# Optimization experiments

Measured on AMD Instinct MI355X. Metric: run time of the kernel, lower is better.

The kernel has to match this reference:

```python
import jax, jax.numpy as jnp
import numpy as np

B, N, C, H = 4, 2048, 384, 8
HD = C // H  # 48; divisible by 6 so RoPE3D splits into three even-sized chunks
ROPE_BASE = 100.0  # RoPE3D(100)


def _rope1d(x, p):
    # x: [B,H,N,d], p: [B,N] integer positions
    d = x.shape[-1]
    inv = 1.0 / (ROPE_BASE ** (jnp.arange(0, d, 2, dtype=jnp.float32) / d))  # [d/2]
    ang = p[:, None, :, None].astype(jnp.float32) * inv                      # [B,1,N,d/2]
    ang = jnp.concatenate([ang, ang], axis=-1)                               # [B,1,N,d]
    cos, sin = jnp.cos(ang), jnp.sin(ang)
    x1, x2 = jnp.split(x, 2, axis=-1)
    return x * cos + jnp.concatenate([-x2, x1], axis=-1) * sin


def _rope3d(x, pos):
    # x: [B,H,N,D], pos: [B,N,3]; rotate each D/3 chunk by one spatial axis
    parts = jnp.split(x, 3, axis=-1)
    return jnp.concatenate([_rope1d(parts[i], pos[..., i]) for i in range(3)], axis=-1)


def setup_inputs() -> dict:
    key = jax.random.key(0)
    ks = jax.random.split(key, 9)
    T = B * N
    s = 1.0 / np.sqrt(C).astype(np.float32)
    offs = jnp.arange(1, B + 1, dtype=jnp.int32) * N  # equal-length segments
    return {
        "query": jax.random.normal(ks[0], (T, C), jnp.float32),
        "key": jax.random.normal(ks[1], (T, C), jnp.float32),
        "value": jax.random.normal(ks[2], (T, C), jnp.float32),
        "Wq": jax.random.normal(ks[3], (C, C), jnp.float32) * s,
        "bq": jnp.zeros((C,), jnp.float32),
        "Wk": jax.random.normal(ks[4], (C, C), jnp.float32) * s,
        "bk": jnp.zeros((C,), jnp.float32),
        "Wv": jax.random.normal(ks[5], (C, C), jnp.float32) * s,
        "bv": jnp.zeros((C,), jnp.float32),
        "Wo": jax.random.normal(ks[6], (C, C), jnp.float32) * s,
        "bo": jnp.zeros((C,), jnp.float32),
        "qpos": jax.random.randint(ks[7], (T, 3), 0, 100),
        "kpos": jax.random.randint(ks[8], (T, 3), 0, 100),
        "src_point_offset": offs,
        "tgt_point_offset": offs,
    }


def reference(query, key, value, Wq, bq, Wk, bk, Wv, bv, Wo, bo,
              qpos, kpos, src_point_offset, tgt_point_offset):
    # Equal-length segments (offsets = [N,2N,...]) => the per-item python loop
    # in forward_pcd_to_pcd is exactly one batched attention over [B,N,C].
    qb = query.reshape(B, N, C)
    kb = key.reshape(B, N, C)
    vb = value.reshape(B, N, C)
    q = (qb @ Wq.T + bq).reshape(B, N, H, HD).transpose(0, 2, 1, 3)  # [B,H,N,HD]
    k = (kb @ Wk.T + bk).reshape(B, N, H, HD).transpose(0, 2, 1, 3)
    v = (vb @ Wv.T + bv).reshape(B, N, H, HD).transpose(0, 2, 1, 3)
    q = _rope3d(q, qpos.reshape(B, N, 3))
    k = _rope3d(k, kpos.reshape(B, N, 3))
    scale = 1.0 / np.sqrt(HD).astype(np.float32)
    attn = jax.nn.softmax(jnp.einsum("bhqd,bhkd->bhqk", q, k) * scale, axis=-1)
    x = jnp.einsum("bhqk,bhkd->bhqd", attn, v)  # [B,H,N,HD]
    x = x.transpose(0, 2, 1, 3).reshape(B * N, C)
    return x @ Wo.T + bo
```

## Files before the change

kernel.cpp:

```cpp
#include <hip/hip_runtime.h>
#include <hip/hip_bf16.h>
#include <math.h>


typedef __attribute__((ext_vector_type(8))) short bf16x8;
typedef __attribute__((ext_vector_type(4))) float f32x4;
typedef __attribute__((ext_vector_type(4))) short s16x4;

__device__ inline short f2bf(float f) {
    unsigned u = __float_as_uint(f);
    u += 0x7fffu + ((u >> 16) & 1u);
    return (short)(u >> 16);
}
__device__ inline unsigned pk_bf16(float a, float b) {
    __hip_bfloat162 h = __float22bfloat162_rn(make_float2(a, b));
    return *(reinterpret_cast<unsigned*>(&h));
}
__device__ inline unsigned pk2(float lo, float hi) {
    return (__float_as_uint(lo) >> 16) | (__float_as_uint(hi) & 0xffff0000u);
}
__device__ inline float bflo(unsigned u) { return __uint_as_float(u << 16); }
__device__ inline float bfhi(unsigned u) { return __uint_as_float(u & 0xffff0000u); }
__device__ inline float exp2f_fast(float x) {
#if __has_builtin(__builtin_amdgcn_exp2f)
    return __builtin_amdgcn_exp2f(x);
#else
    return exp2f(x);
#endif
}
__device__ inline float ffract(float x) {
    float r;
    asm("v_fract_f32 %0, %1" : "=v"(r) : "v"(x));
    return r;
}
__device__ inline float fsin(float x) {
    float r;
    asm("v_sin_f32 %0, %1\n\ts_nop 1" : "=v"(r) : "v"(x));
    return r;
}
__device__ inline float fcos(float x) {
    float r;
    asm("v_cos_f32 %0, %1\n\ts_nop 1" : "=v"(r) : "v"(x));
    return r;
}
__device__ inline int div48(int c) { return (c * 683) >> 15; }

__global__ __launch_bounds__(256)
void cvt_w(const float* __restrict__ w0, const float* __restrict__ w1,
           const float* __restrict__ w2, const float* __restrict__ w3,
           short* __restrict__ Wh, short* __restrict__ Wl)
{
    const float* s = blockIdx.y == 0 ? w0 : blockIdx.y == 1 ? w1
                   : blockIdx.y == 2 ? w2 : w3;
    const size_t i = (size_t)(blockIdx.x * 256 + threadIdx.x) * 4;
    const int c = (int)(i / 384);
    const int k = (int)(i % 384);
    const float4 x = *(const float4*)(s + i);
    const unsigned h01 = pk2(x.x, x.y);
    const unsigned h23 = pk2(x.z, x.w);
    const unsigned l01 = pk2(x.x - bflo(h01), x.y - bfhi(h01));
    const unsigned l23 = pk2(x.z - bflo(h23), x.w - bfhi(h23));
    const size_t off =
        ((((size_t)blockIdx.y * 24 + (c >> 4)) * 12 + (k >> 5)) * 64
         + ((k >> 3) & 3) * 16 + (c & 15)) * 8 + (k & 7);
    uint2 hv; hv.x = h01; hv.y = h23;
    uint2 lv; lv.x = l01; lv.y = l23;
    *(uint2*)(Wh + off) = hv;
    *(uint2*)(Wl + off) = lv;
}

__global__ __launch_bounds__(256, 6)
void gemm_qkv(const float* __restrict__ q_in, const float* __restrict__ k_in,
              const float* __restrict__ v_in,
              const short* __restrict__ Whp, const short* __restrict__ Wlp,
              const float* __restrict__ bq, const float* __restrict__ bk,
              const float* __restrict__ bv,
              const int* __restrict__ qpos, const int* __restrict__ kpos,
              short* __restrict__ qp0, short* __restrict__ qtb,
              short* __restrict__ kp0, short* __restrict__ ktb,
              short* __restrict__ vp)
{
    const int z = blockIdx.z;
    const float* A = z == 0 ? q_in : z == 1 ? k_in : v_in;
    const float* bias = z == 0 ? bq : z == 1 ? bk : bv;

    const int tid = threadIdx.x;
    const int wv = tid >> 6, lane = tid & 63;
    const int l15 = lane & 15, quad = lane >> 4;
    const int mb = blockIdx.x * 32;
    const int nbl = wv * 32;
    const int n0 = blockIdx.y * 128;

    const int tbase = blockIdx.y * 8 + wv * 2 + z * 24;
    const short* wfh = Whp + ((size_t)tbase * 12 * 64 + lane) * 8;
    const short* wfl = Wlp + ((size_t)tbase * 12 * 64 + lane) * 8;

    f32x4 acc[2][2] = {};
    const float* a0 = A + (size_t)(mb + l15) * 384 + quad * 8;

    for (int ks = 0; ks < 12; ++ks) {
        const int o = ks * 32;
        bf16x8 ah[2], al[2];
        #pragma unroll
        for (int mt = 0; mt < 2; ++mt) {
            const float4 x0 = *(const float4*)(a0 + o + mt * 16 * 384);
            const float4 x1 = *(const float4*)(a0 + o + mt * 16 * 384 + 4);
            union { bf16x8 v; unsigned u[4]; } ch, cl;
            ch.u[0] = pk2(x0.x, x0.y);
            ch.u[1] = pk2(x0.z, x0.w);
            ch.u[2] = pk2(x1.x, x1.y);
            ch.u[3] = pk2(x1.z, x1.w);
            cl.u[0] = pk2(x0.x - bflo(ch.u[0]), x0.y - bfhi(ch.u[0]));
            cl.u[1] = pk2(x0.z - bflo(ch.u[1]), x0.w - bfhi(ch.u[1]));
            cl.u[2] = pk2(x1.x - bflo(ch.u[2]), x1.y - bfhi(ch.u[2]));
            cl.u[3] = pk2(x1.z - bflo(ch.u[3]), x1.w - bfhi(ch.u[3]));
            ah[mt] = ch.v;
            al[mt] = cl.v;
        }

        #pragma unroll
        for (int nt = 0; nt < 2; ++nt) {
            const bf16x8 wh = *(const bf16x8*)(wfh + (nt * 12 + ks) * 512);
            const bf16x8 wl = *(const bf16x8*)(wfl + (nt * 12 + ks) * 512);
            #pragma unroll
            for (int mt = 0; mt < 2; ++mt) {
                acc[mt][nt] = __builtin_amdgcn_mfma_f32_16x16x32_bf16(
                    ah[mt], wh, acc[mt][nt], 0, 0, 0);
                acc[mt][nt] = __builtin_amdgcn_mfma_f32_16x16x32_bf16(
                    al[mt], wh, acc[mt][nt], 0, 0, 0);
                acc[mt][nt] = __builtin_amdgcn_mfma_f32_16x16x32_bf16(
                    ah[mt], wl, acc[mt][nt], 0, 0, 0);
            }
        }
    }

    if (z < 2) {
        const int* pos = z ? kpos : qpos;
        const float oscale = z ? 1.0f : 0.2082339551542919f;
        const float invf = exp2f_fast(-(float)(l15 & 7) * 0.8304820237218405f)
                         * 0.15915494309189535f;
        const bool lo_half = (l15 < 8);
        #pragma unroll
        for (int nt = 0; nt < 2; ++nt) {
            const int c = n0 + nbl + nt * 16 + l15;
            const int h = div48(c);
            const int r0 = c - h * 48;
            const int axis = r0 >> 4;
            const float bb = bias[c];
            #pragma unroll
            for (int mt = 0; mt < 2; ++mt) {
                float a[4], pr[4];
                #pragma unroll
                for (int r = 0; r < 4; ++r) a[r] = acc[mt][nt][r] + bb;
                #pragma unroll
                for (int r = 0; r < 4; ++r) pr[r] = __shfl_xor(a[r], 8);
                #pragma unroll
                for (int r = 0; r < 4; ++r) {
                    const int t = mb + mt * 16 + quad * 4 + r;
                    const float pp = (float)pos[t * 3 + axis];
                    const float fr = ffract(pp * invf);
                    const float sn = fsin(fr), cn = fcos(fr);
                    const float o2 = lo_half ? (a[r] * cn - pr[r] * sn)
                                             : (a[r] * cn + pr[r] * sn);
                    const short val = f2bf(o2 * oscale);
                    const int b = t >> 11, n = t & 2047;
                    const int bh_ = b * 8 + h;
                    if (r0 < 32) {
                        short* pbuf = z ? kp0 : qp0;
                        pbuf[(((size_t)bh_ * 128 + (n >> 4)) * 64
                              + (r0 >> 3) * 16 + (n & 15)) * 8 + (r0 & 7)] = val;
                    } else if (z == 0) {
                        const int dd = r0 - 32;
                        qtb[(((size_t)bh_ * 128 + (n >> 4)) * 32
                             + (dd >> 3) * 16 + (n & 15)) * 8 + (dd & 7)] = val;
                    } else {
                        const int dd = r0 - 32;
                        ktb[(((size_t)bh_ * 64 + (n >> 5)) * 64
                             + ((n >> 4) & 1) * 32 + (dd >> 3) * 16 + (n & 15)) * 8
                            + (dd & 7)] = val;
                    }
                }
            }
        }
    } else {
        #pragma unroll
        for (int nt = 0; nt < 2; ++nt) {
            const int c = n0 + nbl + nt * 16 + l15;
            const int h = div48(c);
            const int r0 = c - h * 48;
            const float bb = bias[c];
            #pragma unroll
            for (int mt = 0; mt < 2; ++mt) {
                const int t0 = mb + mt * 16 + quad * 4;
                const int b = t0 >> 11, n = t0 & 2047;
                const int bh_ = b * 8 + h;
                s16x4 pk;
                #pragma unroll
                for (int r = 0; r < 4; ++r)
                    ((short*)&pk)[r] = f2bf(acc[mt][nt][r] + bb);
                const size_t off =
                    ((((size_t)bh_ * 16 + (n >> 7)) * 3 + (r0 >> 4)) * 4
                     + ((n >> 5) & 3)) * 512
                    + (((n >> 3) & 3) * 16 + (r0 & 15)) * 8 + (n & 7);
                *(s16x4*)(vp + off) = pk;
            }
        }
    }
}

__global__ __launch_bounds__(256, 6)
void gemm_out(const short* __restrict__ xh, const short* __restrict__ xl,
              const short* __restrict__ Whp, const short* __restrict__ Wlp,
              const float* __restrict__ bo, float* __restrict__ out)
{
    const int tid = threadIdx.x;
    const int wv = tid >> 6, lane = tid & 63;
    const int l15 = lane & 15, quad = lane >> 4;
    const int mb = blockIdx.x * 16;
    const int nbl = wv * 32;
    const int n0 = blockIdx.y * 128;

    const int tbase = blockIdx.y * 8 + wv * 2 + 3 * 24;
    const short* wfh = Whp + ((size_t)tbase * 12 * 64 + lane) * 8;
    const short* wfl = Wlp + ((size_t)tbase * 12 * 64 + lane) * 8;

    f32x4 acc[2] = {};
    const short* a0 = xh + (size_t)(mb + l15) * 384 + quad * 8;
    const short* a1 = xl + (size_t)(mb + l15) * 384 + quad * 8;

    for (int ks = 0; ks < 12; ++ks) {
        const int o = ks * 32;
        const bf16x8 ah = *(const bf16x8*)(a0 + o);
        const bf16x8 al = *(const bf16x8*)(a1 + o);

        #pragma unroll
        for (int nt = 0; nt < 2; ++nt) {
            const bf16x8 wh = *(const bf16x8*)(wfh + (nt * 12 + ks) * 512);
            const bf16x8 wl = *(const bf16x8*)(wfl + (nt * 12 + ks) * 512);
            acc[nt] = __builtin_amdgcn_mfma_f32_16x16x32_bf16(
                ah, wh, acc[nt], 0, 0, 0);
            acc[nt] = __builtin_amdgcn_mfma_f32_16x16x32_bf16(
                al, wh, acc[nt], 0, 0, 0);
            acc[nt] = __builtin_amdgcn_mfma_f32_16x16x32_bf16(
                ah, wl, acc[nt], 0, 0, 0);
        }
    }

    #pragma unroll
    for (int nt = 0; nt < 2; ++nt) {
        const int c = n0 + nbl + nt * 16 + l15;
        const float bb = bo[c];
        #pragma unroll
        for (int r = 0; r < 4; ++r)
            out[(size_t)(mb + quad * 4 + r) * 384 + c] = acc[nt][r] + bb;
    }
}

__global__ __launch_bounds__(256, 3)
void attn_mfma(const short* __restrict__ Qp0, const short* __restrict__ Qt,
               const short* __restrict__ Kp0, const short* __restrict__ Kt,
               const short* __restrict__ Vp,
               short* __restrict__ x2h, short* __restrict__ x2l)
{
    __shared__ short Stg[24 * 512];
    __shared__ short Ps[4][16][136];
    const int tid = threadIdx.x;
    const int wave = tid >> 6;
    const int lane = tid & 63;
    const int l15 = lane & 15;
    const int quad = lane >> 4;
    const int L = blockIdx.x;
    const int bh = (L & 7) + ((L >> 8) << 3);
    const int q0 = ((L >> 3) & 31) << 6;

    const int qt16 = (q0 >> 4) + wave;
    const bf16x8 qb0 = *(const bf16x8*)
        (Qp0 + (((size_t)bh * 128 + qt16) * 64 + lane) * 8);
    const bf16x8 qtl = *(const bf16x8*)
        (Qt + (((size_t)bh * 128 + qt16) * 32 + (lane & 31)) * 8);
    const bf16x8 z8 = {0, 0, 0, 0, 0, 0, 0, 0};
    const bf16x8 qb1lo = (quad < 2) ? qtl : z8;
    const bf16x8 qb1hi = (quad < 2) ? z8 : qtl;

    f32x4 of[3];
    #pragma unroll
    for (int t = 0; t < 3; ++t) of[t] = (f32x4){0.f, 0.f, 0.f, 0.f};
    f32x4 lsv = (f32x4){0.f, 0.f, 0.f, 0.f};

    const int fbase = wave * 6;

    bf16x8 rs[6];
    #pragma unroll
    for (int i = 0; i < 6; ++i) {
        const int f = fbase + i;
        const short* src;
        if (f < 8)
            src = Kp0 + (((size_t)bh * 128 + f) * 64 + lane) * 8;
        else if (f < 12)
            src = Kt + (((size_t)bh * 64 + (f - 8)) * 64 + lane) * 8;
        else
            src = Vp + ((((size_t)bh * 16) * 12 + (f - 12)) * 64 + lane) * 8;
        rs[i] = *(const bf16x8*)src;
    }

    for (int kt = 0; kt < 16; ++kt) {
        __syncthreads();
        #pragma unroll
        for (int i = 0; i < 6; ++i)
            *(bf16x8*)&Stg[(fbase + i) * 512 + lane * 8] = rs[i];
        __syncthreads();

        if (kt < 15) {
            #pragma unroll
            for (int i = 0; i < 6; ++i) {
                const int f = fbase + i;
                const short* src;
                if (f < 8)
                    src = Kp0 + (((size_t)bh * 128 + (kt + 1) * 8 + f) * 64 + lane) * 8;
                else if (f < 12)
                    src = Kt + (((size_t)bh * 64 + (kt + 1) * 4 + (f - 8)) * 64 + lane) * 8;
                else
                    src = Vp + ((((size_t)bh * 16 + kt + 1) * 12 + (f - 12)) * 64 + lane) * 8;
                rs[i] = *(const bf16x8*)src;
            }
        }

        f32x4 sf[8];
        __builtin_amdgcn_s_setprio(1);
        #pragma unroll
        for (int p = 0; p < 4; ++p) {
            const bf16x8 ka0 = *(const bf16x8*)&Stg[(2 * p) * 512 + lane * 8];
            const bf16x8 ka1 = *(const bf16x8*)&Stg[(2 * p + 1) * 512 + lane * 8];
            const bf16x8 kts = *(const bf16x8*)&Stg[(8 + p) * 512 + lane * 8];
            f32x4 z0 = (f32x4){0.f, 0.f, 0.f, 0.f};
            z0 = __builtin_amdgcn_mfma_f32_16x16x32_bf16(ka0, qb0, z0, 0, 0, 0);
            sf[2 * p] = __builtin_amdgcn_mfma_f32_16x16x32_bf16(kts, qb1lo, z0, 0, 0, 0);
            f32x4 z1 = (f32x4){0.f, 0.f, 0.f, 0.f};
            z1 = __builtin_amdgcn_mfma_f32_16x16x32_bf16(ka1, qb0, z1, 0, 0, 0);
            sf[2 * p + 1] = __builtin_amdgcn_mfma_f32_16x16x32_bf16(kts, qb1hi, z1, 0, 0, 0);
        }
        __builtin_amdgcn_s_setprio(0);

        #pragma unroll
        for (int t = 0; t < 8; ++t) {
            const float p0 = exp2f_fast(sf[t][0]);
            const float p1 = exp2f_fast(sf[t][1]);
            const float p2 = exp2f_fast(sf[t][2]);
            const float p3 = exp2f_fast(sf[t][3]);
            lsv[0] += p0; lsv[1] += p1; lsv[2] += p2; lsv[3] += p3;
            uint2 w;
            w.x = pk_bf16(p0, p1);
            w.y = pk_bf16(p2, p3);
            *(uint2*)&Ps[wave][l15][t * 16 + quad * 4] = w;
        }

        bf16x8 pb[4];
        #pragma unroll
        for (int s = 0; s < 4; ++s)
            pb[s] = *(const bf16x8*)&Ps[wave][l15][s * 32 + quad * 8];
        __builtin_amdgcn_s_setprio(1);
        #pragma unroll
        for (int t = 0; t < 3; ++t) {
            #pragma unroll
            for (int s = 0; s < 4; ++s) {
                const bf16x8 va = *(const bf16x8*)&Stg[(12 + t * 4 + s) * 512 + lane * 8];
                of[t] = __builtin_amdgcn_mfma_f32_16x16x32_bf16(
                    va, pb[s], of[t], 0, 0, 0);
            }
        }
        __builtin_amdgcn_s_setprio(0);
    }

    float ls = (lsv[0] + lsv[1]) + (lsv[2] + lsv[3]);
    ls += __shfl_xor(ls, 16);
    ls += __shfl_xor(ls, 32);
    const float invl = 1.0f / ls;
    const int b = bh >> 3, h = bh & 7;
    const size_t off = (size_t)(b * 2048 + q0 + wave * 16 + l15) * 384
                     + h * 48 + quad * 4;
    #pragma unroll
    for (int t = 0; t < 3; ++t) {
        const float o0 = of[t][0] * invl;
        const float o1 = of[t][1] * invl;
        const float o2 = of[t][2] * invl;
        const float o3 = of[t][3] * invl;
        const unsigned h01 = pk_bf16(o0, o1);
        const unsigned h23 = pk_bf16(o2, o3);
        uint2 hv; hv.x = h01; hv.y = h23;
        uint2 lv;
        lv.x = pk2(o0 - bflo(h01), o1 - bfhi(h01));
        lv.y = pk2(o2 - bflo(h23), o3 - bfhi(h23));
        *(uint2*)(x2h + off + t * 16) = hv;
        *(uint2*)(x2l + off + t * 16) = lv;
    }
}

extern "C" void kernel_launch(void* const* d_in, const int* in_sizes, int n_in,
                              void* d_out, int out_size, void* d_ws, size_t ws_size,
                              hipStream_t stream)
{
    const float* query = (const float*)d_in[0];
    const float* key_  = (const float*)d_in[1];
    const float* value = (const float*)d_in[2];
    const float* Wq = (const float*)d_in[3];
    const float* bq = (const float*)d_in[4];
    const float* Wk = (const float*)d_in[5];
    const float* bk = (const float*)d_in[6];
    const float* Wv = (const float*)d_in[7];
    const float* bv = (const float*)d_in[8];
    const float* Wo = (const float*)d_in[9];
    const float* bo = (const float*)d_in[10];
    const int* qpos = (const int*)d_in[11];
    const int* kpos = (const int*)d_in[12];

    const size_t QP0_S = (size_t)32 * 128 * 64 * 8;
    const size_t QT_S  = (size_t)32 * 128 * 32 * 8;
    const size_t KP0_S = QP0_S;
    const size_t KT_S  = (size_t)32 * 64 * 64 * 8;
    const size_t VP_S  = (size_t)32 * 16 * 12 * 64 * 8;
    const size_t X2_S  = (size_t)8192 * 384;
    const size_t W_S   = (size_t)4 * 384 * 384;

    short* w = (short*)d_ws;
    short* qp0 = w;  w += QP0_S;
    short* qtb = w;  w += QT_S;
    short* kp0 = w;  w += KP0_S;
    short* ktb = w;  w += KT_S;
    short* vp  = w;  w += VP_S;
    short* x2h = w;  w += X2_S;
    short* x2l = w;  w += X2_S;
    short* Wh  = w;  w += W_S;
    short* Wl  = w;

    const dim3 blk(256);
    cvt_w<<<dim3(144, 4), blk, 0, stream>>>(Wq, Wk, Wv, Wo, Wh, Wl);
    gemm_qkv<<<dim3(256, 3, 3), blk, 0, stream>>>(
        query, key_, value, Wh, Wl, bq, bk, bv, qpos, kpos,
        qp0, qtb, kp0, ktb, vp);
    attn_mfma<<<dim3(1024), blk, 0, stream>>>(qp0, qtb, kp0, ktb, vp, x2h, x2l);
    gemm_out<<<dim3(512, 3), blk, 0, stream>>>(x2h, x2l, Wh, Wl, bo,
                                               (float*)d_out);
}
```

Baseline: 252.3 us.

## Enlarge QKV GEMM block tile and prefetch next A k-slice in both projection GEMMs

The QKV projection block now covers 64 rows by 128 columns, arranged as 2x2 waves each computing 32x64, instead of four waves each doing 32x32. This halves the grid and lets each weight fragment load feed more MFMAs. Both the QKV and output GEMMs now software-prefetch the next k-step's A operand into registers before converting and issuing the current step's MFMAs, to hide global load latency. The cost is more registers per thread (launch bounds lowered from 6 to 4 blocks per CU) and fewer blocks available to fill the machine.

```diff
diff --git a/kernel.cpp b/kernel.cpp
--- a/kernel.cpp
+++ b/kernel.cpp
@@ -69,7 +69,7 @@
     *(uint2*)(Wl + off) = lv;
 }
 
-__global__ __launch_bounds__(256, 6)
+__global__ __launch_bounds__(256, 4)
 void gemm_qkv(const float* __restrict__ q_in, const float* __restrict__ k_in,
               const float* __restrict__ v_in,
               const short* __restrict__ Whp, const short* __restrict__ Wlp,
@@ -87,39 +87,55 @@
     const int tid = threadIdx.x;
     const int wv = tid >> 6, lane = tid & 63;
     const int l15 = lane & 15, quad = lane >> 4;
-    const int mb = blockIdx.x * 32;
-    const int nbl = wv * 32;
+    const int mb = blockIdx.x * 64 + (wv & 1) * 32;
+    const int nbl = (wv >> 1) * 64;
     const int n0 = blockIdx.y * 128;
 
-    const int tbase = blockIdx.y * 8 + wv * 2 + z * 24;
+    const int tbase = blockIdx.y * 8 + (wv >> 1) * 4 + z * 24;
     const short* wfh = Whp + ((size_t)tbase * 12 * 64 + lane) * 8;
     const short* wfl = Wlp + ((size_t)tbase * 12 * 64 + lane) * 8;
 
-    f32x4 acc[2][2] = {};
+    f32x4 acc[2][4] = {};
     const float* a0 = A + (size_t)(mb + l15) * 384 + quad * 8;
+
+    float4 nx0[2], nx1[2];
+    #pragma unroll
+    for (int mt = 0; mt < 2; ++mt) {
+        nx0[mt] = *(const float4*)(a0 + mt * 16 * 384);
+        nx1[mt] = *(const float4*)(a0 + mt * 16 * 384 + 4);
+    }
 
     for (int ks = 0; ks < 12; ++ks) {
         const int o = ks * 32;
+        float4 cx0[2], cx1[2];
+        #pragma unroll
+        for (int mt = 0; mt < 2; ++mt) { cx0[mt] = nx0[mt]; cx1[mt] = nx1[mt]; }
+        if (ks < 11) {
+            #pragma unroll
+            for (int mt = 0; mt < 2; ++mt) {
+                nx0[mt] = *(const float4*)(a0 + o + 32 + mt * 16 * 384);
+                nx1[mt] = *(const float4*)(a0 + o + 32 + mt * 16 * 384 + 4);
+            }
+        }
+
         bf16x8 ah[2], al[2];
         #pragma unroll
         for (int mt = 0; mt < 2; ++mt) {
-            const float4 x0 = *(const float4*)(a0 + o + mt * 16 * 384);
-            const float4 x1 = *(const float4*)(a0 + o + mt * 16 * 384 + 4);
             union { bf16x8 v; unsigned u[4]; } ch, cl;
-            ch.u[0] = pk2(x0.x, x0.y);
-            ch.u[1] = pk2(x0.z, x0.w);
-            ch.u[2] = pk2(x1.x, x1.y);
-            ch.u[3] = pk2(x1.z, x1.w);
-            cl.u[0] = pk2(x0.x - bflo(ch.u[0]), x0.y - bfhi(ch.u[0]));
-            cl.u[1] = pk2(x0.z - bflo(ch.u[1]), x0.w - bfhi(ch.u[1]));
-            cl.u[2] = pk2(x1.x - bflo(ch.u[2]), x1.y - bfhi(ch.u[2]));
-            cl.u[3] = pk2(x1.z - bflo(ch.u[3]), x1.w - bfhi(ch.u[3]));
+            ch.u[0] = pk2(cx0[mt].x, cx0[mt].y);
+            ch.u[1] = pk2(cx0[mt].z, cx0[mt].w);
+            ch.u[2] = pk2(cx1[mt].x, cx1[mt].y);
+            ch.u[3] = pk2(cx1[mt].z, cx1[mt].w);
+            cl.u[0] = pk2(cx0[mt].x - bflo(ch.u[0]), cx0[mt].y - bfhi(ch.u[0]));
+            cl.u[1] = pk2(cx0[mt].z - bflo(ch.u[1]), cx0[mt].w - bfhi(ch.u[1]));
+            cl.u[2] = pk2(cx1[mt].x - bflo(ch.u[2]), cx1[mt].y - bfhi(ch.u[2]));
+            cl.u[3] = pk2(cx1[mt].z - bflo(ch.u[3]), cx1[mt].w - bfhi(ch.u[3]));
             ah[mt] = ch.v;
             al[mt] = cl.v;
         }
 
         #pragma unroll
-        for (int nt = 0; nt < 2; ++nt) {
+        for (int nt = 0; nt < 4; ++nt) {
             const bf16x8 wh = *(const bf16x8*)(wfh + (nt * 12 + ks) * 512);
             const bf16x8 wl = *(const bf16x8*)(wfl + (nt * 12 + ks) * 512);
             #pragma unroll
@@ -141,7 +157,7 @@
                          * 0.15915494309189535f;
         const bool lo_half = (l15 < 8);
         #pragma unroll
-        for (int nt = 0; nt < 2; ++nt) {
+        for (int nt = 0; nt < 4; ++nt) {
             const int c = n0 + nbl + nt * 16 + l15;
             const int h = div48(c);
             const int r0 = c - h * 48;
@@ -184,7 +200,7 @@
         }
     } else {
         #pragma unroll
-        for (int nt = 0; nt < 2; ++nt) {
+        for (int nt = 0; nt < 4; ++nt) {
             const int c = n0 + nbl + nt * 16 + l15;
             const int h = div48(c);
             const int r0 = c - h * 48;
@@ -228,10 +244,17 @@
     const short* a0 = xh + (size_t)(mb + l15) * 384 + quad * 8;
     const short* a1 = xl + (size_t)(mb + l15) * 384 + quad * 8;
 
+    bf16x8 nah = *(const bf16x8*)(a0);
+    bf16x8 nal = *(const bf16x8*)(a1);
+
     for (int ks = 0; ks < 12; ++ks) {
         const int o = ks * 32;
-        const bf16x8 ah = *(const bf16x8*)(a0 + o);
-        const bf16x8 al = *(const bf16x8*)(a1 + o);
+        const bf16x8 ah = nah;
+        const bf16x8 al = nal;
+        if (ks < 11) {
+            nah = *(const bf16x8*)(a0 + o + 32);
+            nal = *(const bf16x8*)(a1 + o + 32);
+        }
 
         #pragma unroll
         for (int nt = 0; nt < 2; ++nt) {
@@ -434,7 +457,7 @@
 
     const dim3 blk(256);
     cvt_w<<<dim3(144, 4), blk, 0, stream>>>(Wq, Wk, Wv, Wo, Wh, Wl);
-    gemm_qkv<<<dim3(256, 3, 3), blk, 0, stream>>>(
+    gemm_qkv<<<dim3(128, 3, 3), blk, 0, stream>>>(
         query, key_, value, Wh, Wl, bq, bk, bv, qpos, kpos,
         qp0, qtb, kp0, ktb, vp);
     attn_mfma<<<dim3(1024), blk, 0, stream>>>(qp0, qtb, kp0, ktb, vp, x2h, x2l);
```

Result: faster. 228.5 us (-9.4%).
